# Optimization experiments

Measured on AMD Instinct MI355X. Metric: run time of the kernel, lower is better.

The kernel has to match this reference:

```python
import jax, jax.numpy as jnp
import numpy as np

N_LAYERS = 2
D_MODEL = 1024
EXPAND = 2
D_INNER = EXPAND * D_MODEL   # 2048
D_STATE = 16
D_CONV = 4
DT_RANK = (D_MODEL + 15) // 16  # 64
BATCH = 2
SEQ = 1024


def setup_inputs() -> dict:
    key = jax.random.key(0)
    ks = jax.random.split(key, 8)
    x = jax.random.normal(ks[0], (BATCH, SEQ, D_MODEL), jnp.float32)
    in_proj_w = jax.random.normal(ks[1], (N_LAYERS, 2 * D_INNER, D_MODEL), jnp.float32) * 0.02
    conv_w = jax.random.normal(ks[2], (N_LAYERS, D_INNER, 1, D_CONV), jnp.float32) * 0.2
    conv_b = jnp.zeros((N_LAYERS, D_INNER), jnp.float32)
    x_proj_w = jax.random.normal(ks[3], (N_LAYERS, DT_RANK + 2 * D_STATE, D_INNER), jnp.float32) * 0.02
    dt_proj_w = jax.random.normal(ks[4], (N_LAYERS, D_INNER, DT_RANK), jnp.float32) * 0.1
    # softplus(b) ~ 0.01 -> realistic small dt init
    dt_proj_b = jnp.full((N_LAYERS, D_INNER), float(np.log(np.expm1(0.01))), jnp.float32)
    A_log = jnp.tile(jnp.log(jnp.arange(1, D_STATE + 1, dtype=jnp.float32))[None, None, :], (N_LAYERS, D_INNER, 1))
    D = jnp.ones((N_LAYERS, D_INNER), jnp.float32)
    out_proj_w = jax.random.normal(ks[5], (N_LAYERS, D_MODEL, D_INNER), jnp.float32) * 0.02
    return {
        'x': x, 'in_proj_w': in_proj_w, 'conv_w': conv_w, 'conv_b': conv_b,
        'x_proj_w': x_proj_w, 'dt_proj_w': dt_proj_w, 'dt_proj_b': dt_proj_b,
        'A_log': A_log, 'D': D, 'out_proj_w': out_proj_w,
    }


def _mamba_block(x, W_in, w_c, b_c, W_x, W_dt, b_dt, A_log, Dp, W_out):
    # x: (B, L, d_model)
    xz = jnp.einsum('bld,ed->ble', x, W_in)           # (B, L, 2*d_inner)
    xc, z = jnp.split(xz, 2, axis=-1)
    # causal depthwise conv1d over time
    xc = xc.transpose(0, 2, 1)                         # (B, d_inner, L)
    xc = jax.lax.conv_general_dilated(
        xc, w_c, window_strides=(1,), padding=[(D_CONV - 1, 0)],
        dimension_numbers=('NCH', 'OIH', 'NCH'), feature_group_count=D_INNER,
    ) + b_c[None, :, None]
    u = jax.nn.silu(xc).transpose(0, 2, 1)             # (B, L, d_inner)
    # input-dependent dt, B, C
    x_dbl = jnp.einsum('bld,ed->ble', u, W_x)          # (B, L, dt_rank+2N)
    dt, Bm, Cm = jnp.split(x_dbl, [DT_RANK, DT_RANK + D_STATE], axis=-1)
    delta = jax.nn.softplus(jnp.einsum('blr,dr->bld', dt, W_dt) + b_dt)  # (B, L, d_inner)
    A = -jnp.exp(A_log)                                 # (d_inner, N)
    dA = jnp.exp(jnp.einsum('bld,dn->bldn', delta, A))  # (B, L, d_inner, N)
    dBu = jnp.einsum('bld,bln,bld->bldn', delta, Bm, u) # (B, L, d_inner, N)

    def step(h, inp):
        dA_t, dBu_t, C_t = inp                          # (B,d,N), (B,d,N), (B,N)
        h = dA_t * h + dBu_t
        return h, jnp.einsum('bdn,bn->bd', h, C_t)

    h0 = jnp.zeros((x.shape[0], D_INNER, D_STATE), x.dtype)
    _, ys = jax.lax.scan(step, h0, (dA.transpose(1, 0, 2, 3), dBu.transpose(1, 0, 2, 3), Cm.transpose(1, 0, 2)))
    y = ys.transpose(1, 0, 2) + u * Dp                  # (B, L, d_inner)
    y = y * jax.nn.silu(z)
    return jnp.einsum('bld,od->blo', y, W_out)          # (B, L, d_model)


def _forward(x, in_proj_w, conv_w, conv_b, x_proj_w, dt_proj_w, dt_proj_b, A_log, D, out_proj_w):
    residual = x
    for i in range(N_LAYERS):
        x = _mamba_block(x, in_proj_w[i], conv_w[i], conv_b[i], x_proj_w[i],
                         dt_proj_w[i], dt_proj_b[i], A_log[i], D[i], out_proj_w[i])
    return x + residual


def reference(x, in_proj_w, conv_w, conv_b, x_proj_w, dt_proj_w, dt_proj_b, A_log, D, out_proj_w):
    return _forward(x, in_proj_w, conv_w, conv_b, x_proj_w, dt_proj_w, dt_proj_b, A_log, D, out_proj_w)
```

## Files before the change

kernel.cpp:

```cpp
#include <hip/hip_runtime.h>
#include <hip/hip_bf16.h>

#define NLAYERS 2
#define DMODEL 1024
#define DINNER 2048
#define DSTATE 16
#define DCONV 4
#define DTRANK 64
#define BATCH 2
#define SEQ 1024
#define TOK (BATCH * SEQ)

#define NCHUNK 32
#define CLEN (SEQ / NCHUNK)
#define KSX 8
#define KSO 4

typedef short bf16x8 __attribute__((ext_vector_type(8)));
typedef float f32x4 __attribute__((ext_vector_type(4)));

__device__ __forceinline__ float softplusf(float x) {
    return (x > 20.f) ? x : log1pf(__expf(x));
}
__device__ __forceinline__ float siluf(float x) {
    return x / (1.f + __expf(-x));
}
__device__ __forceinline__ unsigned short f2bf(float f) {
    union { float f; unsigned int u; } v; v.f = f;
    const unsigned int r = (v.u + 0x7FFFu + ((v.u >> 16) & 1u)) >> 16;
    return (unsigned short)r;
}
__device__ __forceinline__ float bf2f(unsigned short s) {
    union { unsigned int u; float f; } v; v.u = ((unsigned int)s) << 16;
    return v.f;
}

__device__ __forceinline__ void cvt8(const float* __restrict__ in,
                                     unsigned short* __restrict__ out, int i) {
    const float4 a = reinterpret_cast<const float4*>(in)[i * 2 + 0];
    const float4 b = reinterpret_cast<const float4*>(in)[i * 2 + 1];
    ushort4 o0, o1;
    o0.x = f2bf(a.x); o0.y = f2bf(a.y); o0.z = f2bf(a.z); o0.w = f2bf(a.w);
    o1.x = f2bf(b.x); o1.y = f2bf(b.y); o1.z = f2bf(b.z); o1.w = f2bf(b.w);
    reinterpret_cast<ushort4*>(out)[i * 2 + 0] = o0;
    reinterpret_cast<ushort4*>(out)[i * 2 + 1] = o1;
}

__global__ __launch_bounds__(256)
void cvt_f32_bf16(const float* __restrict__ in, unsigned short* __restrict__ out,
                  int n8) {
    const int i = blockIdx.x * 256 + threadIdx.x;
    if (i < n8) cvt8(in, out, i);
}

#define WI8 1048576
#define WO8 524288
#define WX8 49152
#define WD8 32768
__global__ __launch_bounds__(256)
void cvt_weights(const float* __restrict__ wi, const float* __restrict__ wo,
                 const float* __restrict__ wx, const float* __restrict__ wd,
                 unsigned short* __restrict__ wi_bf, unsigned short* __restrict__ wo_bf,
                 unsigned short* __restrict__ wx_bf, unsigned short* __restrict__ wd_bf) {
    int i = blockIdx.x * 256 + threadIdx.x;
    if (i < WI8) { cvt8(wi, wi_bf, i); return; }
    i -= WI8;
    if (i < WO8) { cvt8(wo, wo_bf, i); return; }
    i -= WO8;
    if (i < WX8) { cvt8(wx, wx_bf, i); return; }
    i -= WX8;
    if (i < WD8) { cvt8(wd, wd_bf, i); return; }
}

template <int EPI>
__global__ __launch_bounds__(256)
void gemm_bf16(const unsigned short* __restrict__ Ab, int lda,
               const unsigned short* __restrict__ Wb, int ldw,
               void* __restrict__ Cptr, int ldc, int kLen, int Nw,
               size_t cSlice, const float* __restrict__ bias) {
    __shared__ unsigned short As[128 * 32];
    __shared__ unsigned short Bs[128 * 32];
    const int tid = threadIdx.x;
    const int wave = tid >> 6, lane = tid & 63;
    const int wr = wave >> 1, wc = wave & 1;
    const int m0 = blockIdx.y * 128, n0 = blockIdx.x * 128;
    const int kbeg = blockIdx.z * kLen;
    const int r = lane & 15, kq = lane >> 4;

    f32x4 acc[4][4] = {};

    for (int kt = kbeg; kt < kbeg + kLen; kt += 32) {
#pragma unroll
        for (int i = 0; i < 2; ++i) {
            const int chunk = i * 256 + tid;
            const int m = chunk >> 2, kc = chunk & 3;
            __builtin_amdgcn_global_load_lds(
                (const __attribute__((address_space(1))) void*)
                    &Ab[(size_t)(m0 + m) * lda + kt + kc * 8],
                (__attribute__((address_space(3))) void*)&As[chunk * 8], 16, 0, 0);
            const int wrow = min(n0 + m, Nw - 1);
            __builtin_amdgcn_global_load_lds(
                (const __attribute__((address_space(1))) void*)
                    &Wb[(size_t)wrow * ldw + kt + kc * 8],
                (__attribute__((address_space(3))) void*)&Bs[chunk * 8], 16, 0, 0);
        }
        __syncthreads();
        bf16x8 a[4], b[4];
#pragma unroll
        for (int f = 0; f < 4; ++f) {
            a[f] = *reinterpret_cast<const bf16x8*>(&As[(wr * 64 + f * 16 + r) * 32 + kq * 8]);
            b[f] = *reinterpret_cast<const bf16x8*>(&Bs[(wc * 64 + f * 16 + r) * 32 + kq * 8]);
        }
#pragma unroll
        for (int fi = 0; fi < 4; ++fi)
#pragma unroll
            for (int fj = 0; fj < 4; ++fj)
                acc[fi][fj] = __builtin_amdgcn_mfma_f32_16x16x32_bf16(
                    a[fi], b[fj], acc[fi][fj], 0, 0, 0);
        __syncthreads();
    }

    const int cr = lane >> 4, cc = lane & 15;
#pragma unroll
    for (int fi = 0; fi < 4; ++fi)
#pragma unroll
        for (int fj = 0; fj < 4; ++fj)
#pragma unroll
            for (int p = 0; p < 4; ++p) {
                const int m = m0 + wr * 64 + fi * 16 + cr * 4 + p;
                const int n = n0 + wc * 64 + fj * 16 + cc;
                const float v = acc[fi][fj][p];
                if (EPI == 0) {
                    if (n < Nw)
                        ((float*)Cptr)[(size_t)blockIdx.z * cSlice +
                                       (size_t)m * ldc + n] = v;
                } else if (EPI == 1) {
                    ((float*)Cptr)[(size_t)m * ldc + n] = softplusf(v + bias[n]);
                } else {
                    ((unsigned short*)Cptr)[(size_t)blockIdx.z * cSlice +
                                            (size_t)m * ldc + n] = f2bf(v);
                }
            }
}

__global__ __launch_bounds__(256)
void reduce_x(const float* __restrict__ part, float* __restrict__ xdbl,
              unsigned short* __restrict__ dt_bf) {
    const int i = blockIdx.x * 256 + threadIdx.x;
    if (i >= TOK * 96) return;
    float s = 0.f;
#pragma unroll
    for (int k = 0; k < KSX; ++k) s += part[(size_t)k * (TOK * 96) + i];
    xdbl[i] = s;
    const int t = i / 96, c = i - t * 96;
    if (c < DTRANK) dt_bf[t * DTRANK + c] = f2bf(s);
}

template <int MODE>
__global__ __launch_bounds__(256)
void reduce_out(const unsigned short* __restrict__ part,
                const float* __restrict__ resid, void* __restrict__ outp) {
    const int i = blockIdx.x * 256 + threadIdx.x;
    if (i >= TOK * DMODEL / 4) return;
    float s[4] = {0.f, 0.f, 0.f, 0.f};
#pragma unroll
    for (int k = 0; k < KSO; ++k) {
        const ushort4 p = reinterpret_cast<const ushort4*>(
            &part[(size_t)k * (TOK * DMODEL)])[i];
        s[0] += bf2f(p.x); s[1] += bf2f(p.y); s[2] += bf2f(p.z); s[3] += bf2f(p.w);
    }
    if (MODE == 0) {
        ushort4 o;
        o.x = f2bf(s[0]); o.y = f2bf(s[1]); o.z = f2bf(s[2]); o.w = f2bf(s[3]);
        reinterpret_cast<ushort4*>(outp)[i] = o;
    } else {
        const float4 rr = reinterpret_cast<const float4*>(resid)[i];
        float4 o;
        o.x = s[0] + rr.x; o.y = s[1] + rr.y; o.z = s[2] + rr.z; o.w = s[3] + rr.w;
        reinterpret_cast<float4*>(outp)[i] = o;
    }
}

__global__ __launch_bounds__(256)
void conv_silu(const unsigned short* __restrict__ xz_bf,
               const float* __restrict__ cw,
               const float* __restrict__ cb,
               float* __restrict__ u,
               unsigned short* __restrict__ u_bf) {
    const int idx = blockIdx.x * 256 + threadIdx.x;
    const int d = idx & (DINNER - 1);
    const int token = idx >> 11;
    const int l = token & (SEQ - 1);
    float acc = cb[d];
#pragma unroll
    for (int k = 0; k < DCONV; ++k) {
        const int li = l - (DCONV - 1) + k;
        if (li >= 0)
            acc = fmaf(cw[d * DCONV + k],
                       bf2f(xz_bf[(size_t)(token - (DCONV - 1) + k) * (2 * DINNER) + d]),
                       acc);
    }
    const float uv = siluf(acc);
    u[idx] = uv;
    u_bf[idx] = f2bf(uv);
}

__device__ __forceinline__ void load_b16(const float* __restrict__ p, float* B) {
    const float4* bp = reinterpret_cast<const float4*>(p);
    const float4 b0 = bp[0], b1 = bp[1], b2 = bp[2], b3 = bp[3];
    B[0] = b0.x; B[1] = b0.y; B[2] = b0.z; B[3] = b0.w;
    B[4] = b1.x; B[5] = b1.y; B[6] = b1.z; B[7] = b1.w;
    B[8] = b2.x; B[9] = b2.y; B[10] = b2.z; B[11] = b2.w;
    B[12] = b3.x; B[13] = b3.y; B[14] = b3.z; B[15] = b3.w;
}

__global__ __launch_bounds__(256)
void scan_partial(const float* __restrict__ delta,
                  const float* __restrict__ u,
                  const float* __restrict__ xdbl,
                  const float* __restrict__ A_log,
                  float* __restrict__ hbuf,
                  float* __restrict__ Pbuf) {
    const int b = blockIdx.y / NCHUNK;
    const int c = blockIdx.y % NCHUNK;
    const int d = blockIdx.x * 256 + threadIdx.x;
    const int t0 = b * SEQ + c * CLEN;

    float A_dn[16];
    load_b16(&A_log[d * DSTATE], A_dn);
#pragma unroll
    for (int n = 0; n < 16; ++n) A_dn[n] = -__expf(A_dn[n]);

    float h[16], P[16];
#pragma unroll
    for (int n = 0; n < 16; ++n) { h[n] = 0.f; P[n] = 1.f; }

    float dltA, uvA, BA[16];
    float dltB, uvB, BB[16];
    dltA = delta[(size_t)t0 * DINNER + d];
    uvA = u[(size_t)t0 * DINNER + d];
    load_b16(&xdbl[(size_t)t0 * 96 + DTRANK], BA);

#define PSTEP(dlt_, uv_, Bc_)                              \
    {                                                      \
        const float du = (dlt_) * (uv_);                   \
        _Pragma("unroll")                                  \
        for (int n = 0; n < 16; ++n) {                     \
            const float dA = __expf((dlt_) * A_dn[n]);     \
            h[n] = fmaf(dA, h[n], du * Bc_[n]);            \
            P[n] *= dA;                                    \
        }                                                  \
    }

    for (int l = 0; l < CLEN; l += 2) {
        const int t = t0 + l;
        dltB = delta[(size_t)(t + 1) * DINNER + d];
        uvB = u[(size_t)(t + 1) * DINNER + d];
        load_b16(&xdbl[(size_t)(t + 1) * 96 + DTRANK], BB);
        PSTEP(dltA, uvA, BA);
        if (l + 2 < CLEN) {
            dltA = delta[(size_t)(t + 2) * DINNER + d];
            uvA = u[(size_t)(t + 2) * DINNER + d];
            load_b16(&xdbl[(size_t)(t + 2) * 96 + DTRANK], BA);
        }
        PSTEP(dltB, uvB, BB);
    }
#undef PSTEP

    float* hp = &hbuf[((size_t)(b * NCHUNK + c) * DINNER + d) * DSTATE];
    float* Pp = &Pbuf[((size_t)(b * NCHUNK + c) * DINNER + d) * DSTATE];
#pragma unroll
    for (int q = 0; q < 4; ++q) {
        reinterpret_cast<float4*>(hp)[q] = make_float4(h[q*4], h[q*4+1], h[q*4+2], h[q*4+3]);
        reinterpret_cast<float4*>(Pp)[q] = make_float4(P[q*4], P[q*4+1], P[q*4+2], P[q*4+3]);
    }
}

__global__ __launch_bounds__(256)
void scan_combine(float* __restrict__ hbuf, const float* __restrict__ Pbuf) {
    const int gid = blockIdx.x * 256 + threadIdx.x;
    const int b = gid / (DINNER * DSTATE);
    const int dn = gid - b * (DINNER * DSTATE);
    const size_t base = (size_t)b * NCHUNK * DINNER * DSTATE + dn;
    float hi = 0.f;
#pragma unroll
    for (int c = 0; c < NCHUNK; ++c) {
        const size_t idx = base + (size_t)c * (DINNER * DSTATE);
        const float hl = hbuf[idx];
        const float Pc = Pbuf[idx];
        hbuf[idx] = hi;
        hi = fmaf(Pc, hi, hl);
    }
}

__global__ __launch_bounds__(256)
void scan_final(const float* __restrict__ delta,
                const float* __restrict__ u,
                const float* __restrict__ xdbl,
                const unsigned short* __restrict__ xz_bf,
                const float* __restrict__ A_log,
                const float* __restrict__ Dp,
                const float* __restrict__ hbuf,
                unsigned short* __restrict__ yout) {
    const int b = blockIdx.y / NCHUNK;
    const int c = blockIdx.y % NCHUNK;
    const int d = blockIdx.x * 256 + threadIdx.x;
    const int t0 = b * SEQ + c * CLEN;

    float A_dn[16];
    load_b16(&A_log[d * DSTATE], A_dn);
#pragma unroll
    for (int n = 0; n < 16; ++n) A_dn[n] = -__expf(A_dn[n]);
    const float Dd = Dp[d];

    float h[16];
    load_b16(&hbuf[((size_t)(b * NCHUNK + c) * DINNER + d) * DSTATE], h);

    float dltA, uvA, BA[16], CA[16];
    float dltB, uvB, BB[16], CB[16];
    dltA = delta[(size_t)t0 * DINNER + d];
    uvA = u[(size_t)t0 * DINNER + d];
    load_b16(&xdbl[(size_t)t0 * 96 + DTRANK], BA);
    load_b16(&xdbl[(size_t)t0 * 96 + DTRANK + DSTATE], CA);

#define FSTEP(t_, dlt_, uv_, Bc_, Cc_)                          \
    {                                                           \
        const float du = (dlt_) * (uv_);                        \
        _Pragma("unroll")                                       \
        for (int n = 0; n < 16; ++n) {                          \
            const float dA = __expf((dlt_) * A_dn[n]);          \
            h[n] = fmaf(dA, h[n], du * Bc_[n]);                 \
        }                                                       \
        float s0 = 0.f, s1 = 0.f, s2 = 0.f, s3 = 0.f;           \
        _Pragma("unroll")                                       \
        for (int q = 0; q < 4; ++q) {                           \
            s0 = fmaf(h[q*4+0], Cc_[q*4+0], s0);                \
            s1 = fmaf(h[q*4+1], Cc_[q*4+1], s1);                \
            s2 = fmaf(h[q*4+2], Cc_[q*4+2], s2);                \
            s3 = fmaf(h[q*4+3], Cc_[q*4+3], s3);                \
        }                                                       \
        const float zv = bf2f(xz_bf[(size_t)(t_) * (2 * DINNER) + DINNER + d]); \
        const float y = (s0 + s1) + (s2 + s3) + (uv_) * Dd;     \
        yout[(size_t)(t_) * DINNER + d] = f2bf(y * siluf(zv));  \
    }

    for (int l = 0; l < CLEN; l += 2) {
        const int t = t0 + l;
        dltB = delta[(size_t)(t + 1) * DINNER + d];
        uvB = u[(size_t)(t + 1) * DINNER + d];
        load_b16(&xdbl[(size_t)(t + 1) * 96 + DTRANK], BB);
        load_b16(&xdbl[(size_t)(t + 1) * 96 + DTRANK + DSTATE], CB);
        FSTEP(t, dltA, uvA, BA, CA);
        if (l + 2 < CLEN) {
            dltA = delta[(size_t)(t + 2) * DINNER + d];
            uvA = u[(size_t)(t + 2) * DINNER + d];
            load_b16(&xdbl[(size_t)(t + 2) * 96 + DTRANK], BA);
            load_b16(&xdbl[(size_t)(t + 2) * 96 + DTRANK + DSTATE], CA);
        }
        FSTEP(t + 1, dltB, uvB, BB, CB);
    }
#undef FSTEP
}

extern "C" void kernel_launch(void* const* d_in, const int* in_sizes, int n_in,
                              void* d_out, int out_size, void* d_ws, size_t ws_size,
                              hipStream_t stream) {
    const float* x          = (const float*)d_in[0];
    const float* in_proj_w  = (const float*)d_in[1];
    const float* conv_w     = (const float*)d_in[2];
    const float* conv_b     = (const float*)d_in[3];
    const float* x_proj_w   = (const float*)d_in[4];
    const float* dt_proj_w  = (const float*)d_in[5];
    const float* dt_proj_b  = (const float*)d_in[6];
    const float* A_log      = (const float*)d_in[7];
    const float* Dp         = (const float*)d_in[8];
    const float* out_proj_w = (const float*)d_in[9];
    float* out = (float*)d_out;

    float* ws = (float*)d_ws;
    float* hbuf  = ws;
    float* Pbuf  = hbuf  + 2097152;
    float* xpart = Pbuf  + 2097152;
    float* u     = xpart + 1572864;
    float* delta = u     + 4194304;
    float* xdbl  = delta + 4194304;
    unsigned short* opart  = (unsigned short*)(xdbl + 196608);
    unsigned short* wi_bf  = opart + 8388608;
    unsigned short* wo_bf  = wi_bf + 8388608;
    unsigned short* wx_bf  = wo_bf + 4194304;
    unsigned short* wd_bf  = wx_bf + 393216;
    unsigned short* xz_bf  = wd_bf + 262144;
    unsigned short* u_bf   = xz_bf + 8388608;
    unsigned short* act_bf = u_bf  + 4194304;
    unsigned short* y_bf   = act_bf + 2097152;
    unsigned short* dt_bf  = y_bf  + 4194304;

    cvt_weights<<<(WI8 + WO8 + WX8 + WD8 + 255) / 256, 256, 0, stream>>>(
        in_proj_w, out_proj_w, x_proj_w, dt_proj_w, wi_bf, wo_bf, wx_bf, wd_bf);
    cvt_f32_bf16<<<(TOK * DMODEL / 8 + 255) / 256, 256, 0, stream>>>(
        x, act_bf, TOK * DMODEL / 8);

    for (int layer = 0; layer < NLAYERS; ++layer) {
        const unsigned short* Wi = wi_bf + (size_t)layer * (2 * DINNER) * DMODEL;
        const unsigned short* Wo = wo_bf + (size_t)layer * DMODEL * DINNER;
        const unsigned short* Wx = wx_bf + (size_t)layer * 96 * DINNER;
        const unsigned short* Wd = wd_bf + (size_t)layer * DINNER * DTRANK;
        const float* cw = conv_w    + (size_t)layer * DINNER * DCONV;
        const float* cb = conv_b    + (size_t)layer * DINNER;
        const float* bd = dt_proj_b + (size_t)layer * DINNER;
        const float* Al = A_log     + (size_t)layer * DINNER * DSTATE;
        const float* Dl = Dp        + (size_t)layer * DINNER;

        {
            dim3 grid(4096 / 128, TOK / 128, 1);
            gemm_bf16<3><<<grid, 256, 0, stream>>>(act_bf, DMODEL, Wi, DMODEL,
                                                   xz_bf, 2 * DINNER, DMODEL,
                                                   2 * DINNER, 0, nullptr);
        }
        conv_silu<<<(TOK * DINNER) / 256, 256, 0, stream>>>(xz_bf, cw, cb, u, u_bf);
        {
            dim3 grid(1, TOK / 128, KSX);
            gemm_bf16<0><<<grid, 256, 0, stream>>>(u_bf, DINNER, Wx, DINNER,
                                                   xpart, 96, DINNER / KSX, 96,
                                                   (size_t)TOK * 96, nullptr);
            reduce_x<<<(TOK * 96 + 255) / 256, 256, 0, stream>>>(xpart, xdbl, dt_bf);
        }
        {
            dim3 grid(DINNER / 128, TOK / 128, 1);
            gemm_bf16<1><<<grid, 256, 0, stream>>>(dt_bf, DTRANK, Wd, DTRANK,
                                                   delta, DINNER, DTRANK, DINNER,
                                                   0, bd);
        }
        {
            dim3 gridA(DINNER / 256, BATCH * NCHUNK);
            scan_partial<<<gridA, 256, 0, stream>>>(delta, u, xdbl, Al, hbuf, Pbuf);
            scan_combine<<<(BATCH * DINNER * DSTATE) / 256, 256, 0, stream>>>(hbuf, Pbuf);
            scan_final<<<gridA, 256, 0, stream>>>(delta, u, xdbl, xz_bf, Al, Dl,
                                                  hbuf, y_bf);
        }
        {
            dim3 grid(DMODEL / 128, TOK / 128, KSO);
            gemm_bf16<3><<<grid, 256, 0, stream>>>(y_bf, DINNER, Wo, DINNER,
                                                   opart, DMODEL, DINNER / KSO,
                                                   DMODEL, (size_t)TOK * DMODEL,
                                                   nullptr);
            const int nred = TOK * DMODEL / 4;
            if (layer == NLAYERS - 1) {
                reduce_out<1><<<(nred + 255) / 256, 256, 0, stream>>>(opart, x, out);
            } else {
                reduce_out<0><<<(nred + 255) / 256, 256, 0, stream>>>(opart, nullptr,
                                                                      act_bf);
            }
        }
    }
}
```

Before: 354.1 us.

## Split-K in_proj with fused reduce+conv, bf16 delta/u, merged conversion kernels

Splits the in_proj GEMM along K into two bf16 partial slices and adds a kernel that sums them while doing the causal conv and SiLU, writing u and a separate compact z buffer in bf16. Delta is now stored as bf16 from the dt_proj epilogue, and the scan kernels read bf16 delta and u instead of fp32. The x_proj split-K factor is doubled and the input-activation conversion is folded into the weight-conversion launch. The goal is to cut memory traffic and launch count and to raise in_proj occupancy, at the cost of extra partial-sum traffic and lower precision for delta and u.

```diff
diff --git a/kernel.cpp b/kernel.cpp
--- a/kernel.cpp
+++ b/kernel.cpp
@@ -13,8 +13,9 @@
 
 #define NCHUNK 32
 #define CLEN (SEQ / NCHUNK)
-#define KSX 8
+#define KSX 16
 #define KSO 4
+#define KSI 2
 
 typedef short bf16x8 __attribute__((ext_vector_type(8)));
 typedef float f32x4 __attribute__((ext_vector_type(4)));
@@ -46,22 +47,18 @@
     reinterpret_cast<ushort4*>(out)[i * 2 + 1] = o1;
 }
 
-__global__ __launch_bounds__(256)
-void cvt_f32_bf16(const float* __restrict__ in, unsigned short* __restrict__ out,
-                  int n8) {
-    const int i = blockIdx.x * 256 + threadIdx.x;
-    if (i < n8) cvt8(in, out, i);
-}
-
 #define WI8 1048576
 #define WO8 524288
 #define WX8 49152
 #define WD8 32768
-__global__ __launch_bounds__(256)
-void cvt_weights(const float* __restrict__ wi, const float* __restrict__ wo,
-                 const float* __restrict__ wx, const float* __restrict__ wd,
-                 unsigned short* __restrict__ wi_bf, unsigned short* __restrict__ wo_bf,
-                 unsigned short* __restrict__ wx_bf, unsigned short* __restrict__ wd_bf) {
+#define AC8 262144
+__global__ __launch_bounds__(256)
+void cvt_all(const float* __restrict__ wi, const float* __restrict__ wo,
+             const float* __restrict__ wx, const float* __restrict__ wd,
+             const float* __restrict__ xin,
+             unsigned short* __restrict__ wi_bf, unsigned short* __restrict__ wo_bf,
+             unsigned short* __restrict__ wx_bf, unsigned short* __restrict__ wd_bf,
+             unsigned short* __restrict__ act_bf) {
     int i = blockIdx.x * 256 + threadIdx.x;
     if (i < WI8) { cvt8(wi, wi_bf, i); return; }
     i -= WI8;
@@ -70,6 +67,8 @@
     if (i < WX8) { cvt8(wx, wx_bf, i); return; }
     i -= WX8;
     if (i < WD8) { cvt8(wd, wd_bf, i); return; }
+    i -= WD8;
+    if (i < AC8) { cvt8(xin, act_bf, i); return; }
 }
 
 template <int EPI>
@@ -134,13 +133,60 @@
                     if (n < Nw)
                         ((float*)Cptr)[(size_t)blockIdx.z * cSlice +
                                        (size_t)m * ldc + n] = v;
-                } else if (EPI == 1) {
-                    ((float*)Cptr)[(size_t)m * ldc + n] = softplusf(v + bias[n]);
-                } else {
+                } else if (EPI == 3) {
                     ((unsigned short*)Cptr)[(size_t)blockIdx.z * cSlice +
                                             (size_t)m * ldc + n] = f2bf(v);
+                } else {
+                    ((unsigned short*)Cptr)[(size_t)m * ldc + n] =
+                        f2bf(softplusf(v + bias[n]));
                 }
             }
+}
+
+__global__ __launch_bounds__(256)
+void reduce_in_conv(const unsigned short* __restrict__ inpart,
+                    const float* __restrict__ cw,
+                    const float* __restrict__ cb,
+                    unsigned short* __restrict__ u_bf,
+                    unsigned short* __restrict__ z_bf) {
+    const int gid = blockIdx.x * 256 + threadIdx.x;
+    const int d4 = gid & 511;
+    const int t = gid >> 9;
+    const int l = t & (SEQ - 1);
+    const int d0 = d4 * 4;
+    const unsigned short* p0 = inpart;
+    const unsigned short* p1 = inpart + (size_t)TOK * 4096;
+
+    {
+        const ushort4 a = *reinterpret_cast<const ushort4*>(&p0[(size_t)t * 4096 + 2048 + d0]);
+        const ushort4 b = *reinterpret_cast<const ushort4*>(&p1[(size_t)t * 4096 + 2048 + d0]);
+        ushort4 o;
+        o.x = f2bf(bf2f(a.x) + bf2f(b.x));
+        o.y = f2bf(bf2f(a.y) + bf2f(b.y));
+        o.z = f2bf(bf2f(a.z) + bf2f(b.z));
+        o.w = f2bf(bf2f(a.w) + bf2f(b.w));
+        *reinterpret_cast<ushort4*>(&z_bf[(size_t)t * DINNER + d0]) = o;
+    }
+    float acc0 = cb[d0], acc1 = cb[d0 + 1], acc2 = cb[d0 + 2], acc3 = cb[d0 + 3];
+#pragma unroll
+    for (int k = 0; k < DCONV; ++k) {
+        const int li = l - (DCONV - 1) + k;
+        if (li >= 0) {
+            const size_t row = (size_t)(t - (DCONV - 1) + k) * 4096 + d0;
+            const ushort4 a = *reinterpret_cast<const ushort4*>(&p0[row]);
+            const ushort4 b = *reinterpret_cast<const ushort4*>(&p1[row]);
+            acc0 = fmaf(cw[(d0 + 0) * DCONV + k], bf2f(a.x) + bf2f(b.x), acc0);
+            acc1 = fmaf(cw[(d0 + 1) * DCONV + k], bf2f(a.y) + bf2f(b.y), acc1);
+            acc2 = fmaf(cw[(d0 + 2) * DCONV + k], bf2f(a.z) + bf2f(b.z), acc2);
+            acc3 = fmaf(cw[(d0 + 3) * DCONV + k], bf2f(a.w) + bf2f(b.w), acc3);
+        }
+    }
+    ushort4 o;
+    o.x = f2bf(siluf(acc0));
+    o.y = f2bf(siluf(acc1));
+    o.z = f2bf(siluf(acc2));
+    o.w = f2bf(siluf(acc3));
+    *reinterpret_cast<ushort4*>(&u_bf[(size_t)t * DINNER + d0]) = o;
 }
 
 __global__ __launch_bounds__(256)
@@ -181,30 +227,6 @@
     }
 }
 
-__global__ __launch_bounds__(256)
-void conv_silu(const unsigned short* __restrict__ xz_bf,
-               const float* __restrict__ cw,
-               const float* __restrict__ cb,
-               float* __restrict__ u,
-               unsigned short* __restrict__ u_bf) {
-    const int idx = blockIdx.x * 256 + threadIdx.x;
-    const int d = idx & (DINNER - 1);
-    const int token = idx >> 11;
-    const int l = token & (SEQ - 1);
-    float acc = cb[d];
-#pragma unroll
-    for (int k = 0; k < DCONV; ++k) {
-        const int li = l - (DCONV - 1) + k;
-        if (li >= 0)
-            acc = fmaf(cw[d * DCONV + k],
-                       bf2f(xz_bf[(size_t)(token - (DCONV - 1) + k) * (2 * DINNER) + d]),
-                       acc);
-    }
-    const float uv = siluf(acc);
-    u[idx] = uv;
-    u_bf[idx] = f2bf(uv);
-}
-
 __device__ __forceinline__ void load_b16(const float* __restrict__ p, float* B) {
     const float4* bp = reinterpret_cast<const float4*>(p);
     const float4 b0 = bp[0], b1 = bp[1], b2 = bp[2], b3 = bp[3];
@@ -215,8 +237,8 @@
 }
 
 __global__ __launch_bounds__(256)
-void scan_partial(const float* __restrict__ delta,
-                  const float* __restrict__ u,
+void scan_partial(const unsigned short* __restrict__ delta_bf,
+                  const unsigned short* __restrict__ u_bf,
                   const float* __restrict__ xdbl,
                   const float* __restrict__ A_log,
                   float* __restrict__ hbuf,
@@ -237,8 +259,8 @@
 
     float dltA, uvA, BA[16];
     float dltB, uvB, BB[16];
-    dltA = delta[(size_t)t0 * DINNER + d];
-    uvA = u[(size_t)t0 * DINNER + d];
+    dltA = bf2f(delta_bf[(size_t)t0 * DINNER + d]);
+    uvA = bf2f(u_bf[(size_t)t0 * DINNER + d]);
     load_b16(&xdbl[(size_t)t0 * 96 + DTRANK], BA);
 
 #define PSTEP(dlt_, uv_, Bc_)                              \
@@ -254,13 +276,13 @@
 
     for (int l = 0; l < CLEN; l += 2) {
         const int t = t0 + l;
-        dltB = delta[(size_t)(t + 1) * DINNER + d];
-        uvB = u[(size_t)(t + 1) * DINNER + d];
+        dltB = bf2f(delta_bf[(size_t)(t + 1) * DINNER + d]);
+        uvB = bf2f(u_bf[(size_t)(t + 1) * DINNER + d]);
         load_b16(&xdbl[(size_t)(t + 1) * 96 + DTRANK], BB);
         PSTEP(dltA, uvA, BA);
         if (l + 2 < CLEN) {
-            dltA = delta[(size_t)(t + 2) * DINNER + d];
-            uvA = u[(size_t)(t + 2) * DINNER + d];
+            dltA = bf2f(delta_bf[(size_t)(t + 2) * DINNER + d]);
+            uvA = bf2f(u_bf[(size_t)(t + 2) * DINNER + d]);
             load_b16(&xdbl[(size_t)(t + 2) * 96 + DTRANK], BA);
         }
         PSTEP(dltB, uvB, BB);
@@ -294,10 +316,10 @@
 }
 
 __global__ __launch_bounds__(256)
-void scan_final(const float* __restrict__ delta,
-                const float* __restrict__ u,
+void scan_final(const unsigned short* __restrict__ delta_bf,
+                const unsigned short* __restrict__ u_bf,
                 const float* __restrict__ xdbl,
-                const unsigned short* __restrict__ xz_bf,
+                const unsigned short* __restrict__ z_bf,
                 const float* __restrict__ A_log,
                 const float* __restrict__ Dp,
                 const float* __restrict__ hbuf,
@@ -318,8 +340,8 @@
 
     float dltA, uvA, BA[16], CA[16];
     float dltB, uvB, BB[16], CB[16];
-    dltA = delta[(size_t)t0 * DINNER + d];
-    uvA = u[(size_t)t0 * DINNER + d];
+    dltA = bf2f(delta_bf[(size_t)t0 * DINNER + d]);
+    uvA = bf2f(u_bf[(size_t)t0 * DINNER + d]);
     load_b16(&xdbl[(size_t)t0 * 96 + DTRANK], BA);
     load_b16(&xdbl[(size_t)t0 * 96 + DTRANK + DSTATE], CA);
 
@@ -339,21 +361,21 @@
             s2 = fmaf(h[q*4+2], Cc_[q*4+2], s2);                \
             s3 = fmaf(h[q*4+3], Cc_[q*4+3], s3);                \
         }                                                       \
-        const float zv = bf2f(xz_bf[(size_t)(t_) * (2 * DINNER) + DINNER + d]); \
+        const float zv = bf2f(z_bf[(size_t)(t_) * DINNER + d]); \
         const float y = (s0 + s1) + (s2 + s3) + (uv_) * Dd;     \
         yout[(size_t)(t_) * DINNER + d] = f2bf(y * siluf(zv));  \
     }
 
     for (int l = 0; l < CLEN; l += 2) {
         const int t = t0 + l;
-        dltB = delta[(size_t)(t + 1) * DINNER + d];
-        uvB = u[(size_t)(t + 1) * DINNER + d];
+        dltB = bf2f(delta_bf[(size_t)(t + 1) * DINNER + d]);
+        uvB = bf2f(u_bf[(size_t)(t + 1) * DINNER + d]);
         load_b16(&xdbl[(size_t)(t + 1) * 96 + DTRANK], BB);
         load_b16(&xdbl[(size_t)(t + 1) * 96 + DTRANK + DSTATE], CB);
         FSTEP(t, dltA, uvA, BA, CA);
         if (l + 2 < CLEN) {
-            dltA = delta[(size_t)(t + 2) * DINNER + d];
-            uvA = u[(size_t)(t + 2) * DINNER + d];
+            dltA = bf2f(delta_bf[(size_t)(t + 2) * DINNER + d]);
+            uvA = bf2f(u_bf[(size_t)(t + 2) * DINNER + d]);
             load_b16(&xdbl[(size_t)(t + 2) * 96 + DTRANK], BA);
             load_b16(&xdbl[(size_t)(t + 2) * 96 + DTRANK + DSTATE], CA);
         }
@@ -381,24 +403,23 @@
     float* hbuf  = ws;
     float* Pbuf  = hbuf  + 2097152;
     float* xpart = Pbuf  + 2097152;
-    float* u     = xpart + 1572864;
-    float* delta = u     + 4194304;
-    float* xdbl  = delta + 4194304;
-    unsigned short* opart  = (unsigned short*)(xdbl + 196608);
+    float* xdbl  = xpart + 3145728;
+    unsigned short* inpart = (unsigned short*)(xdbl + 196608);
+    unsigned short* opart  = inpart + 16777216;
     unsigned short* wi_bf  = opart + 8388608;
     unsigned short* wo_bf  = wi_bf + 8388608;
     unsigned short* wx_bf  = wo_bf + 4194304;
     unsigned short* wd_bf  = wx_bf + 393216;
-    unsigned short* xz_bf  = wd_bf + 262144;
-    unsigned short* u_bf   = xz_bf + 8388608;
-    unsigned short* act_bf = u_bf  + 4194304;
+    unsigned short* u_bf   = wd_bf + 262144;
+    unsigned short* z_bf   = u_bf  + 4194304;
+    unsigned short* dlt_bf = z_bf  + 4194304;
+    unsigned short* act_bf = dlt_bf + 4194304;
     unsigned short* y_bf   = act_bf + 2097152;
     unsigned short* dt_bf  = y_bf  + 4194304;
 
-    cvt_weights<<<(WI8 + WO8 + WX8 + WD8 + 255) / 256, 256, 0, stream>>>(
-        in_proj_w, out_proj_w, x_proj_w, dt_proj_w, wi_bf, wo_bf, wx_bf, wd_bf);
-    cvt_f32_bf16<<<(TOK * DMODEL / 8 + 255) / 256, 256, 0, stream>>>(
-        x, act_bf, TOK * DMODEL / 8);
+    cvt_all<<<(WI8 + WO8 + WX8 + WD8 + AC8 + 255) / 256, 256, 0, stream>>>(
+        in_proj_w, out_proj_w, x_proj_w, dt_proj_w, x,
+        wi_bf, wo_bf, wx_bf, wd_bf, act_bf);
 
     for (int layer = 0; layer < NLAYERS; ++layer) {
         const unsigned short* Wi = wi_bf + (size_t)layer * (2 * DINNER) * DMODEL;
@@ -412,12 +433,14 @@
         const float* Dl = Dp        + (size_t)layer * DINNER;
 
         {
-            dim3 grid(4096 / 128, TOK / 128, 1);
+            dim3 grid(4096 / 128, TOK / 128, KSI);
             gemm_bf16<3><<<grid, 256, 0, stream>>>(act_bf, DMODEL, Wi, DMODEL,
-                                                   xz_bf, 2 * DINNER, DMODEL,
-                                                   2 * DINNER, 0, nullptr);
-        }
-        conv_silu<<<(TOK * DINNER) / 256, 256, 0, stream>>>(xz_bf, cw, cb, u, u_bf);
+                                                   inpart, 2 * DINNER,
+                                                   DMODEL / KSI, 2 * DINNER,
+                                                   (size_t)TOK * 4096, nullptr);
+        }
+        reduce_in_conv<<<(TOK * 512) / 256, 256, 0, stream>>>(inpart, cw, cb,
+                                                              u_bf, z_bf);
         {
             dim3 grid(1, TOK / 128, KSX);
             gemm_bf16<0><<<grid, 256, 0, stream>>>(u_bf, DINNER, Wx, DINNER,
@@ -427,16 +450,17 @@
         }
         {
             dim3 grid(DINNER / 128, TOK / 128, 1);
-            gemm_bf16<1><<<grid, 256, 0, stream>>>(dt_bf, DTRANK, Wd, DTRANK,
-                                                   delta, DINNER, DTRANK, DINNER,
+            gemm_bf16<4><<<grid, 256, 0, stream>>>(dt_bf, DTRANK, Wd, DTRANK,
+                                                   dlt_bf, DINNER, DTRANK, DINNER,
                                                    0, bd);
         }
         {
             dim3 gridA(DINNER / 256, BATCH * NCHUNK);
-            scan_partial<<<gridA, 256, 0, stream>>>(delta, u, xdbl, Al, hbuf, Pbuf);
+            scan_partial<<<gridA, 256, 0, stream>>>(dlt_bf, u_bf, xdbl, Al,
+                                                    hbuf, Pbuf);
             scan_combine<<<(BATCH * DINNER * DSTATE) / 256, 256, 0, stream>>>(hbuf, Pbuf);
-            scan_final<<<gridA, 256, 0, stream>>>(delta, u, xdbl, xz_bf, Al, Dl,
-                                                  hbuf, y_bf);
+            scan_final<<<gridA, 256, 0, stream>>>(dlt_bf, u_bf, xdbl, z_bf,
+                                                  Al, Dl, hbuf, y_bf);
         }
         {
             dim3 grid(DMODEL / 128, TOK / 128, KSO);
```

After: 385.4 us. 8.9% more time.
